# Kernel optimization log

Measured on AMD Instinct MI355X. Metric: run time of the kernel, lower is better.

Reference implementation:

```python
import jax, jax.numpy as jnp
import numpy as np
from jax import lax

B, T, F, H, NC = 64, 256, 64, 128, 2


def setup_inputs() -> dict:
    key = jax.random.key(0)
    ks = jax.random.split(key, 10)
    # timestamps: sorted ints with duplicates -> exercises per-timestamp mean aggregation
    t = jnp.sort(jax.random.randint(ks[0], (B, T), 0, T // 2), axis=1).astype(jnp.float32)
    m = jax.random.randint(ks[1], (B, T), 0, F).astype(jnp.float32)
    x = jax.random.normal(ks[2], (B, T), dtype=jnp.float32)
    delt = jax.random.uniform(ks[3], (B, T), dtype=jnp.float32)
    X = jnp.stack([t, m, x, delt], axis=1)  # [B, 4, T]
    lengths = jax.random.randint(ks[4], (B,), T // 2, T + 1).astype(jnp.int32)
    s = 1.0 / np.sqrt(H + 1)
    W_lin = jax.random.uniform(ks[5], (F, H + 1, 4 * H), minval=-s, maxval=s, dtype=jnp.float32)
    b_lin = jax.random.uniform(ks[6], (F, 4 * H), minval=-s, maxval=s, dtype=jnp.float32)
    W_dec = jax.random.uniform(ks[7], (F,), minval=-1.0, maxval=1.0, dtype=jnp.float32)
    b_dec = jax.random.uniform(ks[8], (F,), minval=-1.0, maxval=1.0, dtype=jnp.float32)
    so = 1.0 / np.sqrt(F * H + H)
    k9, k10 = jax.random.split(ks[9])
    W_out = jax.random.uniform(k9, (F * H + H, NC), minval=-so, maxval=so, dtype=jnp.float32)
    b_out = jax.random.uniform(k10, (NC,), minval=-so, maxval=so, dtype=jnp.float32)
    return {"X": X, "lengths": lengths, "W_lin": W_lin, "b_lin": b_lin,
            "W_dec": W_dec, "b_dec": b_dec, "W_out": W_out, "b_out": b_out}


def _forward(X, lengths, W_lin, b_lin, W_dec, b_dec, W_out, b_out):
    nF, Hp1, H4 = W_lin.shape
    hs = Hp1 - 1
    t = X[:, 0]
    m = X[:, 1].astype(jnp.int32)
    x = X[:, 2]
    delt = X[:, 3]
    idx = jnp.arange(t.shape[1])
    valid = idx[None, :] < lengths[:, None]                       # event is real
    t_next = jnp.concatenate([t[:, 1:], t[:, -1:] + 1.0], axis=1)
    # last event of a consecutive-equal-timestamp group (within valid length)
    boundary = (idx[None, :] == (lengths[:, None] - 1)) | (t_next != t)

    def per_sample(m_s, x_s, d_s, v_s, b_s):
        def step(carry, inp):
            h_t, c_t, acc, cnt = carry
            mj, xj, dj, vj, bj = inp
            # feature-specific decay of that feature's hidden row
            dm = W_dec[mj] * dj + b_dec[mj]
            decay = jnp.exp(-jnp.maximum(0.0, dm))
            h_dec = decay * h_t[mj]
            inp_vec = jnp.concatenate([xj[None], h_dec])          # [H+1]
            gates = inp_vec @ W_lin[mj] + b_lin[mj]               # [4H]
            gi, gf, go, gc = jnp.split(gates, 4)
            c_cand = jax.nn.sigmoid(gf) * c_t + jax.nn.sigmoid(gi) * jnp.tanh(gc)
            h_row = jax.nn.sigmoid(go) * jnp.tanh(c_cand)
            h_t = jnp.where(vj, h_t.at[mj].set(h_row), h_t)
            acc = acc + jnp.where(vj, c_cand, 0.0)
            cnt = cnt + jnp.where(vj, 1.0, 0.0)
            close = vj & bj                                       # end of timestamp group
            c_t = jnp.where(close, acc / jnp.maximum(cnt, 1.0), c_t)
            acc = jnp.where(close, jnp.zeros_like(acc), acc)
            cnt = jnp.where(close, 0.0, cnt)
            return (h_t, c_t, acc, cnt), None

        init = (jnp.zeros((nF, hs), jnp.float32), jnp.zeros((hs,), jnp.float32),
                jnp.zeros((hs,), jnp.float32), jnp.float32(0.0))
        (h_t, c_t, _, _), _ = lax.scan(step, init, (m_s, x_s, d_s, v_s, b_s))
        feats = jnp.concatenate([c_t, h_t.reshape(-1)])           # [H + F*H]
        return jax.nn.softmax(feats @ W_out + b_out)

    return jax.vmap(per_sample)(m, x, delt, valid, boundary)      # [B, n_class]


def reference(X, lengths, W_lin, b_lin, W_dec, b_dec, W_out, b_out):
    return _forward(X, lengths, W_lin, b_lin, W_dec, b_dec, W_out, b_out)
```

## Files before the change

kernel.cpp:

```cpp
#include <hip/hip_runtime.h>
#include <math.h>
#include <stdint.h>

#define BATCH 64
#define T 256
#define NF 64
#define H 128
#define H4 512
#define HP1 129
#define WF_STRIDE (HP1 * H4)
#define FEATS (NF * H + H)
#define NTH 1024

#define PACK8_U4 (64 * 2 * 2 * 1024)
#define PACK8_BYTES ((size_t)PACK8_U4 * 16u)

typedef _Float16 half2_t __attribute__((ext_vector_type(2)));
typedef float    vf2     __attribute__((ext_vector_type(2)));

__device__ __forceinline__ float sigmoidf_(float x) {
    return 1.0f / (1.0f + __expf(-x));
}

__device__ __forceinline__ float tanhf_(float x) {
    float ax = fabsf(x);
    float e = __expf(2.0f * ax);
    float r = 1.0f - 2.0f / (e + 1.0f);
    return copysignf(r, x);
}

__device__ __forceinline__ float fdot2_(half2_t a, half2_t b, float c) {
#if defined(__has_builtin)
#if __has_builtin(__builtin_amdgcn_fdot2)
    return __builtin_amdgcn_fdot2(a, b, c, false);
#else
    return fmaf((float)a.x, (float)b.x, fmaf((float)a.y, (float)b.y, c));
#endif
#else
    return fmaf((float)a.x, (float)b.x, fmaf((float)a.y, (float)b.y, c));
#endif
}

template<bool HI>
__device__ __forceinline__ half2_t dec8(unsigned u) {
    vf2 f = __builtin_amdgcn_cvt_pk_f32_fp8(u, HI);
    return (half2_t)__builtin_amdgcn_cvt_pkrtz(f[0], f[1]);
}

__global__ __launch_bounds__(256)
void repack8_kernel(const float* __restrict__ W_lin, uint4* __restrict__ pack) {
    const int lin = blockIdx.x * 256 + threadIdx.x;
    const int tid = lin & 1023;
    const int q   = (lin >> 10) & 1;
    const int h   = (lin >> 11) & 1;
    const int f   = lin >> 12;
    const int kh  = tid >> 9;
    const int cc  = tid & 511;
    const int k0  = h * 64 + kh * 32 + q * 16;
    const float* src = W_lin + (size_t)f * WF_STRIDE + (size_t)(1 + k0) * H4 + cc;
    unsigned u[4];
    #pragma unroll
    for (int w = 0; w < 4; ++w) {
        const float v0 = src[(4 * w + 0) * H4] * 4096.0f;
        const float v1 = src[(4 * w + 1) * H4] * 4096.0f;
        const float v2 = src[(4 * w + 2) * H4] * 4096.0f;
        const float v3 = src[(4 * w + 3) * H4] * 4096.0f;
        unsigned r = 0;
        r = __builtin_amdgcn_cvt_pk_fp8_f32(v0, v1, r, false);
        r = __builtin_amdgcn_cvt_pk_fp8_f32(v2, v3, r, true);
        u[w] = r;
    }
    uint4 o; o.x = u[0]; o.y = u[1]; o.z = u[2]; o.w = u[3];
    pack[lin] = o;
}

__global__ __launch_bounds__(NTH, 4)
void lstm_scan_fp8_kernel(const float* __restrict__ X,
                          const int* __restrict__ lengths,
                          const float* __restrict__ W_lin,
                          const float* __restrict__ b_lin,
                          const float* __restrict__ W_dec,
                          const float* __restrict__ b_dec,
                          const float* __restrict__ W_out,
                          const float* __restrict__ b_out,
                          const uint4* __restrict__ pack,
                          float* __restrict__ out)
{
    __shared__ float s_feats[FEATS];
    __shared__ half2_t s_inp2[H / 2];
    __shared__ float s_part[2][H4];
    __shared__ float s_X[4 * T];
    __shared__ float s_wdec[NF];
    __shared__ float s_bdec[NF];
    __shared__ float s_red[32];

    float* s_ct = s_feats;
    float* s_ht = s_feats + H;

    const int tid = threadIdx.x;
    const int b   = blockIdx.x;
    const int c   = tid & 511;
    const int kh  = tid >> 9;

    const float* Xb = X + b * 4 * T;
    const int len = lengths[b];

    for (int i = tid; i < NF * H; i += NTH) s_ht[i] = 0.0f;
    for (int i = tid; i < 4 * T; i += NTH) s_X[i] = Xb[i];
    if (tid < NF) { s_wdec[tid] = W_dec[tid]; s_bdec[tid] = b_dec[tid]; }
    if (tid < H / 2) { half2_t z; z.x = (_Float16)0.0f; z.y = (_Float16)0.0f; s_inp2[tid] = z; }
    __syncthreads();

    float c_t = 0.0f, acc = 0.0f, cnt = 0.0f;

    #define DOTU4(W, IB) do {                                                   \
        const half2_t* ip = ((const half2_t*)s_inp2) + (IB);                    \
        union { uint4 u; half2_t h[4]; } I0, I1;                                \
        I0.u = *(const uint4*)(ip);                                             \
        I1.u = *(const uint4*)(ip + 4);                                         \
        a = fdot2_(dec8<false>(W.x), I0.h[0], a);                               \
        a = fdot2_(dec8<true >(W.x), I0.h[1], a);                               \
        a = fdot2_(dec8<false>(W.y), I0.h[2], a);                               \
        a = fdot2_(dec8<true >(W.y), I0.h[3], a);                               \
        a = fdot2_(dec8<false>(W.z), I1.h[0], a);                               \
        a = fdot2_(dec8<true >(W.z), I1.h[1], a);                               \
        a = fdot2_(dec8<false>(W.w), I1.h[2], a);                               \
        a = fdot2_(dec8<true >(W.w), I1.h[3], a);                               \
    } while (0)

    uint4 A0a, A0b, B0a, B0b;
    float4 blA = make_float4(0.f, 0.f, 0.f, 0.f), blB = make_float4(0.f, 0.f, 0.f, 0.f);
    float  wxA = 0.0f, wxB = 0.0f;

    {
        const int m0 = (int)s_X[T];
        const uint4* p0 = pack + (size_t)(m0 * 2) * 2048;
        A0a = p0[tid]; A0b = p0[1024 + tid];
        if (tid < H) {
            const float* bb = b_lin + m0 * H4 + tid;
            blA.x = bb[0]; blA.y = bb[H]; blA.z = bb[2 * H]; blA.w = bb[3 * H];
        }
        if (kh == 0) wxA = W_lin[(size_t)m0 * WF_STRIDE + c];
    }

    #define STEP(C0A, C0B, N0A, N0B, CBL, NBL, CWX, NWX)                        \
    {                                                                           \
        const int   mj  = (int)s_X[T + j];                                      \
        const float xj  = s_X[2 * T + j];                                       \
        const int   jn  = (j + 1 < T) ? (j + 1) : (T - 1);                      \
        const int   mjn = (int)s_X[T + jn];                                     \
                                                 \
        const uint4* p1 = pack + (size_t)(mj * 2 + 1) * 2048;                   \
        const uint4 h1a = p1[tid];                                              \
        const uint4 h1b = p1[1024 + tid];                                       \
                            \
        const uint4* p0n = pack + (size_t)(mjn * 2) * 2048;                     \
        N0A = p0n[tid]; N0B = p0n[1024 + tid];                                  \
        if (tid < H) {                                                          \
            const float* bb = b_lin + mjn * H4 + tid;                           \
            NBL.x = bb[0]; NBL.y = bb[H]; NBL.z = bb[2 * H]; NBL.w = bb[3 * H]; \
        }                                                                       \
        if (kh == 0) NWX = W_lin[(size_t)mjn * WF_STRIDE + c];                  \
               \
        float a = 0.0f;                                                         \
        DOTU4(C0A, kh * 16);                                                    \
        DOTU4(C0B, kh * 16 + 8);                                                \
        DOTU4(h1a, 32 + kh * 16);                                               \
        DOTU4(h1b, 32 + kh * 16 + 8);                                           \
        a *= (1.0f / 4096.0f);                                                  \
        if (kh == 0) a = fmaf(xj, CWX, a);                                      \
        s_part[kh][c] = a;                                                      \
        __syncthreads();                                 \
        if (tid < H) {                                                          \
            const int h = tid;                                                  \
            const float gi = s_part[0][h]       + s_part[1][h]       + CBL.x;   \
            const float gf = s_part[0][H + h]   + s_part[1][H + h]   + CBL.y;   \
            const float go = s_part[0][2*H + h] + s_part[1][2*H + h] + CBL.z;   \
            const float gc = s_part[0][3*H + h] + s_part[1][3*H + h] + CBL.w;   \
            const float c_cand = sigmoidf_(gf) * c_t + sigmoidf_(gi) * tanhf_(gc); \
            const float h_row  = sigmoidf_(go) * tanhf_(c_cand);                \
            s_ht[mj * H + h] = h_row;                                           \
            acc += c_cand;                                                      \
            cnt += 1.0f;                                                        \
            const float tj = s_X[j];                                            \
            const float tn = (j < T - 1) ? s_X[j + 1] : (tj + 1.0f);            \
            const bool boundary = (j == len - 1) || (tn != tj);                 \
            if (boundary) { c_t = acc / fmaxf(cnt, 1.0f); acc = 0.0f; cnt = 0.0f; } \
                                  \
            const float dn  = s_X[3 * T + jn];                                  \
            const float dmn = fmaf(s_wdec[mjn], dn, s_bdec[mjn]);               \
            const float den = __expf(-fmaxf(0.0f, dmn));                        \
            const float hv  = (mjn == mj) ? h_row : s_ht[mjn * H + h];          \
            ((_Float16*)s_inp2)[h] = (_Float16)(den * hv);                      \
        }                                                                       \
        __syncthreads();                             \
    }

    int j = 0;
    while (j < len) {
        STEP(A0a, A0b, B0a, B0b, blA, blB, wxA, wxB); ++j;
        if (j >= len) break;
        STEP(B0a, B0b, A0a, A0b, blB, blA, wxB, wxA); ++j;
    }
    #undef STEP
    #undef DOTU4

    if (tid < H) s_ct[tid] = c_t;
    __syncthreads();

    float z0 = 0.0f, z1 = 0.0f;
    for (int i = tid; i < FEATS; i += NTH) {
        const float f = s_feats[i];
        const float2 w = *(const float2*)(W_out + 2 * i);
        z0 = fmaf(f, w.x, z0);
        z1 = fmaf(f, w.y, z1);
    }
    #pragma unroll
    for (int off = 32; off > 0; off >>= 1) {
        z0 += __shfl_down(z0, off, 64);
        z1 += __shfl_down(z1, off, 64);
    }
    const int wave = tid >> 6, lane = tid & 63;
    if (lane == 0) { s_red[2 * wave] = z0; s_red[2 * wave + 1] = z1; }
    __syncthreads();
    if (tid == 0) {
        float a0 = b_out[0], a1 = b_out[1];
        #pragma unroll
        for (int w = 0; w < 16; ++w) { a0 += s_red[2 * w]; a1 += s_red[2 * w + 1]; }
        const float mx = fmaxf(a0, a1);
        const float e0 = __expf(a0 - mx), e1 = __expf(a1 - mx);
        const float inv = 1.0f / (e0 + e1);
        out[2 * b]     = e0 * inv;
        out[2 * b + 1] = e1 * inv;
    }
}

#define NTHREADS 512
__global__ __launch_bounds__(NTHREADS)
void lstm_scan_kernel(const float* __restrict__ X,
                      const int* __restrict__ lengths,
                      const float* __restrict__ W_lin,
                      const float* __restrict__ b_lin,
                      const float* __restrict__ W_dec,
                      const float* __restrict__ b_dec,
                      const float* __restrict__ W_out,
                      const float* __restrict__ b_out,
                      float* __restrict__ out)
{
    __shared__ float s_feats[FEATS];
    __shared__ float s_inp[H];
    __shared__ float s_part[4][H4];
    __shared__ float s_X[4 * T];
    __shared__ float s_wdec[NF];
    __shared__ float s_bdec[NF];
    __shared__ float s_red[16];

    float* s_ct = s_feats;
    float* s_ht = s_feats + H;

    const int tid = threadIdx.x;
    const int b   = blockIdx.x;
    const int g4  = tid & 127;
    const int kq  = tid >> 7;

    const float* Xb = X + b * 4 * T;
    const int len = lengths[b];

    for (int i = tid; i < NF * H; i += NTHREADS) s_ht[i] = 0.0f;
    for (int i = tid; i < 4 * T; i += NTHREADS) s_X[i] = Xb[i];
    if (tid < NF) { s_wdec[tid] = W_dec[tid]; s_bdec[tid] = b_dec[tid]; }
    __syncthreads();

    float c_t = 0.0f, acc = 0.0f, cnt = 0.0f;

    for (int j = 0; j < len; ++j) {
        const int   mj = (int)s_X[T + j];
        const float xj = s_X[2 * T + j];
        const float* Wf = W_lin + mj * WF_STRIDE;

        float bl0, bl1, bl2, bl3;
        if (tid < H) {
            const float dj    = s_X[3 * T + j];
            const float dm    = fmaf(s_wdec[mj], dj, s_bdec[mj]);
            const float decay = __expf(-fmaxf(0.0f, dm));
            s_inp[tid] = decay * s_ht[mj * H + tid];
            const int m4 = mj * H4;
            bl0 = b_lin[m4 + tid];
            bl1 = b_lin[m4 + H + tid];
            bl2 = b_lin[m4 + 2 * H + tid];
            bl3 = b_lin[m4 + 3 * H + tid];
        }
        __syncthreads();

        float4 a4 = make_float4(0.0f, 0.0f, 0.0f, 0.0f);
        {
            const float*  wr  = Wf + (1 + kq * 32) * H4 + 4 * g4;
            const float4* ivp = (const float4*)(s_inp + kq * 32);
            #pragma unroll
            for (int cc = 0; cc < 8; ++cc) {
                const float4 v = ivp[cc];
                const float* wrc = wr + (4 * cc) * H4;
                const float4 w0 = *(const float4*)(wrc);
                const float4 w1 = *(const float4*)(wrc + H4);
                const float4 w2 = *(const float4*)(wrc + 2 * H4);
                const float4 w3 = *(const float4*)(wrc + 3 * H4);
                a4.x = fmaf(v.x, w0.x, a4.x); a4.y = fmaf(v.x, w0.y, a4.y);
                a4.z = fmaf(v.x, w0.z, a4.z); a4.w = fmaf(v.x, w0.w, a4.w);
                a4.x = fmaf(v.y, w1.x, a4.x); a4.y = fmaf(v.y, w1.y, a4.y);
                a4.z = fmaf(v.y, w1.z, a4.z); a4.w = fmaf(v.y, w1.w, a4.w);
                a4.x = fmaf(v.z, w2.x, a4.x); a4.y = fmaf(v.z, w2.y, a4.y);
                a4.z = fmaf(v.z, w2.z, a4.z); a4.w = fmaf(v.z, w2.w, a4.w);
                a4.x = fmaf(v.w, w3.x, a4.x); a4.y = fmaf(v.w, w3.y, a4.y);
                a4.z = fmaf(v.w, w3.z, a4.z); a4.w = fmaf(v.w, w3.w, a4.w);
            }
        }
        if (kq == 0) {
            const float4 w = *(const float4*)(Wf + 4 * g4);
            a4.x = fmaf(xj, w.x, a4.x); a4.y = fmaf(xj, w.y, a4.y);
            a4.z = fmaf(xj, w.z, a4.z); a4.w = fmaf(xj, w.w, a4.w);
        }
        *(float4*)(&s_part[kq][4 * g4]) = a4;
        __syncthreads();

        if (tid < H) {
            const int h = tid;
            const float gi = s_part[0][h]         + s_part[1][h]         + s_part[2][h]         + s_part[3][h]         + bl0;
            const float gf = s_part[0][H + h]     + s_part[1][H + h]     + s_part[2][H + h]     + s_part[3][H + h]     + bl1;
            const float go = s_part[0][2*H + h]   + s_part[1][2*H + h]   + s_part[2][2*H + h]   + s_part[3][2*H + h]   + bl2;
            const float gc = s_part[0][3*H + h]   + s_part[1][3*H + h]   + s_part[2][3*H + h]   + s_part[3][3*H + h]   + bl3;

            const float c_cand = sigmoidf_(gf) * c_t + sigmoidf_(gi) * tanhf_(gc);
            const float h_row  = sigmoidf_(go) * tanhf_(c_cand);
            s_ht[mj * H + h] = h_row;
            acc += c_cand;
            cnt += 1.0f;

            const float tj = s_X[j];
            const float tn = (j < T - 1) ? s_X[j + 1] : (tj + 1.0f);
            const bool boundary = (j == len - 1) || (tn != tj);
            if (boundary) { c_t = acc / fmaxf(cnt, 1.0f); acc = 0.0f; cnt = 0.0f; }
        }
        __syncthreads();
    }

    if (tid < H) s_ct[tid] = c_t;
    __syncthreads();

    float z0 = 0.0f, z1 = 0.0f;
    for (int i = tid; i < FEATS; i += NTHREADS) {
        const float f = s_feats[i];
        const float2 w = *(const float2*)(W_out + 2 * i);
        z0 = fmaf(f, w.x, z0);
        z1 = fmaf(f, w.y, z1);
    }
    #pragma unroll
    for (int off = 32; off > 0; off >>= 1) {
        z0 += __shfl_down(z0, off, 64);
        z1 += __shfl_down(z1, off, 64);
    }
    const int wave = tid >> 6, lane = tid & 63;
    if (lane == 0) { s_red[2 * wave] = z0; s_red[2 * wave + 1] = z1; }
    __syncthreads();
    if (tid == 0) {
        float a0 = b_out[0], a1 = b_out[1];
        #pragma unroll
        for (int w = 0; w < 8; ++w) { a0 += s_red[2 * w]; a1 += s_red[2 * w + 1]; }
        const float mx = fmaxf(a0, a1);
        const float e0 = __expf(a0 - mx), e1 = __expf(a1 - mx);
        const float inv = 1.0f / (e0 + e1);
        out[2 * b]     = e0 * inv;
        out[2 * b + 1] = e1 * inv;
    }
}

extern "C" void kernel_launch(void* const* d_in, const int* in_sizes, int n_in,
                              void* d_out, int out_size, void* d_ws, size_t ws_size,
                              hipStream_t stream) {
    const float* X      = (const float*)d_in[0];
    const int*   lens   = (const int*)d_in[1];
    const float* W_lin  = (const float*)d_in[2];
    const float* b_lin  = (const float*)d_in[3];
    const float* W_dec  = (const float*)d_in[4];
    const float* b_dec  = (const float*)d_in[5];
    const float* W_out  = (const float*)d_in[6];
    const float* b_out  = (const float*)d_in[7];
    float* out = (float*)d_out;

    if (ws_size >= PACK8_BYTES) {
        uint4* pack = (uint4*)d_ws;
        hipLaunchKernelGGL(repack8_kernel, dim3(PACK8_U4 / 256), dim3(256), 0, stream,
                           W_lin, pack);
        hipLaunchKernelGGL(lstm_scan_fp8_kernel, dim3(BATCH), dim3(NTH), 0, stream,
                           X, lens, W_lin, b_lin, W_dec, b_dec, W_out, b_out, pack, out);
    } else {
        hipLaunchKernelGGL(lstm_scan_kernel, dim3(BATCH), dim3(NTHREADS), 0, stream,
                           X, lens, W_lin, b_lin, W_dec, b_dec, W_out, b_out, out);
    }
}
```

Baseline: 465.7 us.

## Stream FP8 weights into an LDS ring via direct global-to-LDS DMA

Replaces register-held weight prefetch with asynchronous global_load_lds transfers into a three-slot LDS ring buffer. The next feature's weights are issued while the current step's dot products run, with explicit vmcnt waits. Row 0 of W_lin and b_lin are packed into an fp16 header table and DMA'd the same way, and the pack layout is reordered per wave. Two accumulators break the fdot2 dependency chain. The gain is better latency hiding on the serial scan, at the cost of more LDS, hand-written waitcnt/barrier sequencing, an extra prep kernel, and fp16 rounding of the bias and input weights.

```diff
diff --git a/kernel.cpp b/kernel.cpp
--- a/kernel.cpp
+++ b/kernel.cpp
@@ -12,8 +12,11 @@
 #define FEATS (NF * H + H)
 #define NTH 1024
 
-#define PACK8_U4 (64 * 2 * 2 * 1024)
+#define RING_HALF 32768
+#define PACK8_U4 (64 * 16 * 4 * 64)
 #define PACK8_BYTES ((size_t)PACK8_U4 * 16u)
+#define HDR_BYTES  (64u * 1024u * 2u)
+#define WS_NEED ((size_t)HDR_BYTES + PACK8_BYTES)
 
 typedef _Float16 half2_t __attribute__((ext_vector_type(2)));
 typedef float    vf2     __attribute__((ext_vector_type(2)));
@@ -47,24 +50,44 @@
     return (half2_t)__builtin_amdgcn_cvt_pkrtz(f[0], f[1]);
 }
 
+__device__ __forceinline__ void dma16(const void* g, uint32_t lds_byte) {
+    __builtin_amdgcn_global_load_lds(
+        (const __attribute__((address_space(1))) void*)g,
+        (__attribute__((address_space(3))) void*)(uintptr_t)lds_byte,
+        16, 0, 0);
+}
+__device__ __forceinline__ void dma4(const void* g, uint32_t lds_byte) {
+    __builtin_amdgcn_global_load_lds(
+        (const __attribute__((address_space(1))) void*)g,
+        (__attribute__((address_space(3))) void*)(uintptr_t)lds_byte,
+        4, 0, 0);
+}
+
+#define WAITV(N) do { asm volatile("s_waitcnt vmcnt(" #N ")" ::: "memory"); \
+                      __builtin_amdgcn_sched_barrier(0); } while (0)
+#define BARRIER() do { asm volatile("s_waitcnt lgkmcnt(0)" ::: "memory"); \
+                       __builtin_amdgcn_s_barrier(); \
+                       asm volatile("" ::: "memory"); } while (0)
+
 __global__ __launch_bounds__(256)
 void repack8_kernel(const float* __restrict__ W_lin, uint4* __restrict__ pack) {
     const int lin = blockIdx.x * 256 + threadIdx.x;
-    const int tid = lin & 1023;
-    const int q   = (lin >> 10) & 1;
-    const int h   = (lin >> 11) & 1;
+    const int l   = lin & 63;
+    const int i   = (lin >> 6) & 3;
+    const int wv  = (lin >> 8) & 15;
     const int f   = lin >> 12;
+    const int tid = wv * 64 + l;
     const int kh  = tid >> 9;
     const int cc  = tid & 511;
-    const int k0  = h * 64 + kh * 32 + q * 16;
-    const float* src = W_lin + (size_t)f * WF_STRIDE + (size_t)(1 + k0) * H4 + cc;
+    const int k0  = kh * 64 + i * 16;
     unsigned u[4];
     #pragma unroll
     for (int w = 0; w < 4; ++w) {
-        const float v0 = src[(4 * w + 0) * H4] * 4096.0f;
-        const float v1 = src[(4 * w + 1) * H4] * 4096.0f;
-        const float v2 = src[(4 * w + 2) * H4] * 4096.0f;
-        const float v3 = src[(4 * w + 3) * H4] * 4096.0f;
+        const float* src = W_lin + (size_t)f * WF_STRIDE + (size_t)(1 + k0 + 4 * w) * H4 + cc;
+        const float v0 = src[0]      * 4096.0f;
+        const float v1 = src[H4]     * 4096.0f;
+        const float v2 = src[2 * H4] * 4096.0f;
+        const float v3 = src[3 * H4] * 4096.0f;
         unsigned r = 0;
         r = __builtin_amdgcn_cvt_pk_fp8_f32(v0, v1, r, false);
         r = __builtin_amdgcn_cvt_pk_fp8_f32(v2, v3, r, true);
@@ -74,33 +97,44 @@
     pack[lin] = o;
 }
 
+__global__ __launch_bounds__(256)
+void hdr_kernel(const float* __restrict__ W_lin, const float* __restrict__ b_lin,
+                _Float16* __restrict__ hdr) {
+    const int lin = blockIdx.x * 256 + threadIdx.x;
+    const int f = lin >> 10, t = lin & 1023;
+    const float v = (t < 512) ? W_lin[(size_t)f * WF_STRIDE + t]
+                              : b_lin[f * H4 + (t & 511)];
+    hdr[lin] = (_Float16)v;
+}
+
 __global__ __launch_bounds__(NTH, 4)
-void lstm_scan_fp8_kernel(const float* __restrict__ X,
-                          const int* __restrict__ lengths,
-                          const float* __restrict__ W_lin,
-                          const float* __restrict__ b_lin,
-                          const float* __restrict__ W_dec,
-                          const float* __restrict__ b_dec,
-                          const float* __restrict__ W_out,
-                          const float* __restrict__ b_out,
-                          const uint4* __restrict__ pack,
-                          float* __restrict__ out)
+void lstm_scan_fp8_dma(const float* __restrict__ X,
+                       const int* __restrict__ lengths,
+                       const float* __restrict__ W_dec,
+                       const float* __restrict__ b_dec,
+                       const float* __restrict__ W_out,
+                       const float* __restrict__ b_out,
+                       const uint4* __restrict__ pack,
+                       const _Float16* __restrict__ hdr,
+                       float* __restrict__ out)
 {
-    __shared__ float s_feats[FEATS];
+    __shared__ __align__(16) char s_wb[3 * RING_HALF];
+    __shared__ __align__(16) char s_hd[2 * 4096];
     __shared__ half2_t s_inp2[H / 2];
+    __shared__ float s_ht[NF * H];
     __shared__ float s_part[2][H4];
     __shared__ float s_X[4 * T];
     __shared__ float s_wdec[NF];
     __shared__ float s_bdec[NF];
+    __shared__ float s_cfin[H];
     __shared__ float s_red[32];
 
-    float* s_ct = s_feats;
-    float* s_ht = s_feats + H;
-
-    const int tid = threadIdx.x;
-    const int b   = blockIdx.x;
-    const int c   = tid & 511;
-    const int kh  = tid >> 9;
+    const int tid  = threadIdx.x;
+    const int b    = blockIdx.x;
+    const int wv   = tid >> 6;
+    const int lane = tid & 63;
+    const int kh   = tid >> 9;
+    const int c    = tid & 511;
 
     const float* Xb = X + b * 4 * T;
     const int len = lengths[b];
@@ -108,109 +142,125 @@
     for (int i = tid; i < NF * H; i += NTH) s_ht[i] = 0.0f;
     for (int i = tid; i < 4 * T; i += NTH) s_X[i] = Xb[i];
     if (tid < NF) { s_wdec[tid] = W_dec[tid]; s_bdec[tid] = b_dec[tid]; }
-    if (tid < H / 2) { half2_t z; z.x = (_Float16)0.0f; z.y = (_Float16)0.0f; s_inp2[tid] = z; }
-    __syncthreads();
+    if (tid < H) ((_Float16*)s_inp2)[tid] = (_Float16)0.0f;
+    __syncthreads();
+
+    const uint32_t wb0 = (uint32_t)(uintptr_t)s_wb;
+    const uint32_t hd0 = (uint32_t)(uintptr_t)s_hd;
+    const uint32_t wb_wave = __builtin_amdgcn_readfirstlane(wb0 + wv * 2048);
+    const uint32_t hd_wave = __builtin_amdgcn_readfirstlane(hd0 + wv * 256);
 
     float c_t = 0.0f, acc = 0.0f, cnt = 0.0f;
+
+    #define ISSUE_W(mf, i, slot) do {                                           \
+        const uint4* gp = pack + (((size_t)(mf) * 16 + wv) * 4 + (i)) * 64 + lane; \
+        dma16(gp, wb_wave + (uint32_t)(slot) * RING_HALF + ((i) & 1) * 1024);   \
+    } while (0)
+
+    #define ISSUE_HDR(jj) do {                                                  \
+        const int ss = ((jj) < T) ? (jj) : (T - 1);                             \
+        const _Float16* gh = hdr + (int)s_X[T + ss] * 1024 + (tid & 1022);      \
+        dma4(gh, hd_wave + (((jj) & 1) ? 4096u : 0u));                          \
+    } while (0)
 
     #define DOTU4(W, IB) do {                                                   \
         const half2_t* ip = ((const half2_t*)s_inp2) + (IB);                    \
         union { uint4 u; half2_t h[4]; } I0, I1;                                \
         I0.u = *(const uint4*)(ip);                                             \
         I1.u = *(const uint4*)(ip + 4);                                         \
-        a = fdot2_(dec8<false>(W.x), I0.h[0], a);                               \
-        a = fdot2_(dec8<true >(W.x), I0.h[1], a);                               \
-        a = fdot2_(dec8<false>(W.y), I0.h[2], a);                               \
-        a = fdot2_(dec8<true >(W.y), I0.h[3], a);                               \
-        a = fdot2_(dec8<false>(W.z), I1.h[0], a);                               \
-        a = fdot2_(dec8<true >(W.z), I1.h[1], a);                               \
-        a = fdot2_(dec8<false>(W.w), I1.h[2], a);                               \
-        a = fdot2_(dec8<true >(W.w), I1.h[3], a);                               \
+        a0 = fdot2_(dec8<false>(W.x), I0.h[0], a0);                             \
+        a1 = fdot2_(dec8<true >(W.x), I0.h[1], a1);                             \
+        a0 = fdot2_(dec8<false>(W.y), I0.h[2], a0);                             \
+        a1 = fdot2_(dec8<true >(W.y), I0.h[3], a1);                             \
+        a0 = fdot2_(dec8<false>(W.z), I1.h[0], a0);                             \
+        a1 = fdot2_(dec8<true >(W.z), I1.h[1], a1);                             \
+        a0 = fdot2_(dec8<false>(W.w), I1.h[2], a0);                             \
+        a1 = fdot2_(dec8<true >(W.w), I1.h[3], a1);                             \
     } while (0)
 
-    uint4 A0a, A0b, B0a, B0b;
-    float4 blA = make_float4(0.f, 0.f, 0.f, 0.f), blB = make_float4(0.f, 0.f, 0.f, 0.f);
-    float  wxA = 0.0f, wxB = 0.0f;
+    #define HALF_DOT(slot, hh) do {                                             \
+        const char* bp = s_wb + (size_t)(slot) * RING_HALF + wv * 2048 + lane * 16; \
+        const uint4 W0 = *(const uint4*)(bp);                                   \
+        const uint4 W1 = *(const uint4*)(bp + 1024);                            \
+        DOTU4(W0, kh * 32 + 16 * (hh));                                         \
+        DOTU4(W1, kh * 32 + 16 * (hh) + 8);                                     \
+    } while (0)
 
     {
         const int m0 = (int)s_X[T];
-        const uint4* p0 = pack + (size_t)(m0 * 2) * 2048;
-        A0a = p0[tid]; A0b = p0[1024 + tid];
+        ISSUE_W(m0, 0, 0); ISSUE_W(m0, 1, 0);
+        ISSUE_HDR(0);
+        ISSUE_W(m0, 2, 1); ISSUE_W(m0, 3, 1);
+    }
+
+    int r0 = 0;
+    for (int j = 0; j < len; ++j) {
+        const int   mj  = (int)s_X[T + j];
+        const float xj  = s_X[2 * T + j];
+        const int   jn  = (j + 1 < T) ? (j + 1) : (T - 1);
+        const int   mjn = (int)s_X[T + jn];
+        int r1 = r0 + 1; if (r1 >= 3) r1 -= 3;
+        int r2 = r0 + 2; if (r2 >= 3) r2 -= 3;
+
+        ISSUE_W(mjn, 0, r2); ISSUE_W(mjn, 1, r2);
+        ISSUE_HDR(j + 1);
+        WAITV(5);
+
+        float a0 = 0.0f, a1 = 0.0f;
+        HALF_DOT(r0, 0);
+        asm volatile("s_waitcnt lgkmcnt(0)" ::: "memory");
+        __builtin_amdgcn_sched_barrier(0);
+        ISSUE_W(mjn, 2, r0); ISSUE_W(mjn, 3, r0);
+        WAITV(5);
+        HALF_DOT(r1, 1);
+
+        float a = (a0 + a1) * (1.0f / 4096.0f);
+        {
+            const float hv = (float)*(const _Float16*)(s_hd
+                + ((j & 1) ? 4096 : 0) + wv * 256 + lane * 4 + (tid & 1) * 2);
+            a = kh ? (a + hv) : fmaf(xj, hv, a);
+        }
+        s_part[kh][c] = a;
+        BARRIER();
+
         if (tid < H) {
-            const float* bb = b_lin + m0 * H4 + tid;
-            blA.x = bb[0]; blA.y = bb[H]; blA.z = bb[2 * H]; blA.w = bb[3 * H];
-        }
-        if (kh == 0) wxA = W_lin[(size_t)m0 * WF_STRIDE + c];
-    }
-
-    #define STEP(C0A, C0B, N0A, N0B, CBL, NBL, CWX, NWX)                        \
-    {                                                                           \
-        const int   mj  = (int)s_X[T + j];                                      \
-        const float xj  = s_X[2 * T + j];                                       \
-        const int   jn  = (j + 1 < T) ? (j + 1) : (T - 1);                      \
-        const int   mjn = (int)s_X[T + jn];                                     \
-                                                 \
-        const uint4* p1 = pack + (size_t)(mj * 2 + 1) * 2048;                   \
-        const uint4 h1a = p1[tid];                                              \
-        const uint4 h1b = p1[1024 + tid];                                       \
-                            \
-        const uint4* p0n = pack + (size_t)(mjn * 2) * 2048;                     \
-        N0A = p0n[tid]; N0B = p0n[1024 + tid];                                  \
-        if (tid < H) {                                                          \
-            const float* bb = b_lin + mjn * H4 + tid;                           \
-            NBL.x = bb[0]; NBL.y = bb[H]; NBL.z = bb[2 * H]; NBL.w = bb[3 * H]; \
-        }                                                                       \
-        if (kh == 0) NWX = W_lin[(size_t)mjn * WF_STRIDE + c];                  \
-               \
-        float a = 0.0f;                                                         \
-        DOTU4(C0A, kh * 16);                                                    \
-        DOTU4(C0B, kh * 16 + 8);                                                \
-        DOTU4(h1a, 32 + kh * 16);                                               \
-        DOTU4(h1b, 32 + kh * 16 + 8);                                           \
-        a *= (1.0f / 4096.0f);                                                  \
-        if (kh == 0) a = fmaf(xj, CWX, a);                                      \
-        s_part[kh][c] = a;                                                      \
-        __syncthreads();                                 \
-        if (tid < H) {                                                          \
-            const int h = tid;                                                  \
-            const float gi = s_part[0][h]       + s_part[1][h]       + CBL.x;   \
-            const float gf = s_part[0][H + h]   + s_part[1][H + h]   + CBL.y;   \
-            const float go = s_part[0][2*H + h] + s_part[1][2*H + h] + CBL.z;   \
-            const float gc = s_part[0][3*H + h] + s_part[1][3*H + h] + CBL.w;   \
-            const float c_cand = sigmoidf_(gf) * c_t + sigmoidf_(gi) * tanhf_(gc); \
-            const float h_row  = sigmoidf_(go) * tanhf_(c_cand);                \
-            s_ht[mj * H + h] = h_row;                                           \
-            acc += c_cand;                                                      \
-            cnt += 1.0f;                                                        \
-            const float tj = s_X[j];                                            \
-            const float tn = (j < T - 1) ? s_X[j + 1] : (tj + 1.0f);            \
-            const bool boundary = (j == len - 1) || (tn != tj);                 \
-            if (boundary) { c_t = acc / fmaxf(cnt, 1.0f); acc = 0.0f; cnt = 0.0f; } \
-                                  \
-            const float dn  = s_X[3 * T + jn];                                  \
-            const float dmn = fmaf(s_wdec[mjn], dn, s_bdec[mjn]);               \
-            const float den = __expf(-fmaxf(0.0f, dmn));                        \
-            const float hv  = (mjn == mj) ? h_row : s_ht[mjn * H + h];          \
-            ((_Float16*)s_inp2)[h] = (_Float16)(den * hv);                      \
-        }                                                                       \
-        __syncthreads();                             \
-    }
-
-    int j = 0;
-    while (j < len) {
-        STEP(A0a, A0b, B0a, B0b, blA, blB, wxA, wxB); ++j;
-        if (j >= len) break;
-        STEP(B0a, B0b, A0a, A0b, blB, blA, wxB, wxA); ++j;
-    }
-    #undef STEP
+            const int h = tid;
+            const float gi = s_part[0][h]         + s_part[1][h];
+            const float gf = s_part[0][H + h]     + s_part[1][H + h];
+            const float go = s_part[0][2 * H + h] + s_part[1][2 * H + h];
+            const float gc = s_part[0][3 * H + h] + s_part[1][3 * H + h];
+            const float c_cand = sigmoidf_(gf) * c_t + sigmoidf_(gi) * tanhf_(gc);
+            const float h_row  = sigmoidf_(go) * tanhf_(c_cand);
+            s_ht[mj * H + h] = h_row;
+            acc += c_cand;
+            cnt += 1.0f;
+            const float tj = s_X[j];
+            const float tn = (j < T - 1) ? s_X[j + 1] : (tj + 1.0f);
+            const bool boundary = (j == len - 1) || (tn != tj);
+            if (boundary) { c_t = acc / fmaxf(cnt, 1.0f); acc = 0.0f; cnt = 0.0f; }
+            const float dn  = s_X[3 * T + jn];
+            const float dmn = fmaf(s_wdec[mjn], dn, s_bdec[mjn]);
+            const float den = __expf(-fmaxf(0.0f, dmn));
+            const float hv2 = (mjn == mj) ? h_row : s_ht[mjn * H + h];
+            ((_Float16*)s_inp2)[h] = (_Float16)(den * hv2);
+        }
+        BARRIER();
+        r0 = r2;
+    }
+    #undef HALF_DOT
     #undef DOTU4
-
-    if (tid < H) s_ct[tid] = c_t;
+    #undef ISSUE_HDR
+    #undef ISSUE_W
+
+    asm volatile("s_waitcnt vmcnt(0) lgkmcnt(0)" ::: "memory");
+    __syncthreads();
+
+    if (tid < H) s_cfin[tid] = c_t;
     __syncthreads();
 
     float z0 = 0.0f, z1 = 0.0f;
     for (int i = tid; i < FEATS; i += NTH) {
-        const float f = s_feats[i];
+        const float f = (i < H) ? s_cfin[i] : s_ht[i - H];
         const float2 w = *(const float2*)(W_out + 2 * i);
         z0 = fmaf(f, w.x, z0);
         z1 = fmaf(f, w.y, z1);
@@ -220,8 +270,8 @@
         z0 += __shfl_down(z0, off, 64);
         z1 += __shfl_down(z1, off, 64);
     }
-    const int wave = tid >> 6, lane = tid & 63;
-    if (lane == 0) { s_red[2 * wave] = z0; s_red[2 * wave + 1] = z1; }
+    const int wave = tid >> 6, lane2 = tid & 63;
+    if (lane2 == 0) { s_red[2 * wave] = z0; s_red[2 * wave + 1] = z1; }
     __syncthreads();
     if (tid == 0) {
         float a0 = b_out[0], a1 = b_out[1];
@@ -386,12 +436,14 @@
     const float* b_out  = (const float*)d_in[7];
     float* out = (float*)d_out;
 
-    if (ws_size >= PACK8_BYTES) {
-        uint4* pack = (uint4*)d_ws;
+    if (ws_size >= WS_NEED) {
+        _Float16* hdr = (_Float16*)d_ws;
+        uint4* pack = (uint4*)((char*)d_ws + HDR_BYTES);
         hipLaunchKernelGGL(repack8_kernel, dim3(PACK8_U4 / 256), dim3(256), 0, stream,
                            W_lin, pack);
-        hipLaunchKernelGGL(lstm_scan_fp8_kernel, dim3(BATCH), dim3(NTH), 0, stream,
-                           X, lens, W_lin, b_lin, W_dec, b_dec, W_out, b_out, pack, out);
+        hipLaunchKernelGGL(hdr_kernel, dim3(256), dim3(256), 0, stream, W_lin, b_lin, hdr);
+        hipLaunchKernelGGL(lstm_scan_fp8_dma, dim3(BATCH), dim3(NTH), 0, stream,
+                           X, lens, W_dec, b_dec, W_out, b_out, pack, hdr, out);
     } else {
         hipLaunchKernelGGL(lstm_scan_kernel, dim3(BATCH), dim3(NTHREADS), 0, stream,
                            X, lens, W_lin, b_lin, W_dec, b_dec, W_out, b_out, out);
```

Measured after the change: 493.1 us. +5.9%, slower.
